# Optimization experiments

Hardware: AMD Instinct MI355X
Metric: run time of the kernel (lower is better)

## Reference

```python
import jax, jax.numpy as jnp
import numpy as np

H = 12          # num_attention_heads
HD = 64         # head_dim
GAMMA = 0.5
LOCAL_EPS = 0.8
N_APPROX = 7


def _l1norm(x, axis):
    # torch.nn.functional.normalize(x, p=1, dim=axis)
    n = jnp.sum(jnp.abs(x), axis=axis, keepdims=True)
    return x / jnp.maximum(n, 1e-12)


def setup_inputs() -> dict:
    key = jax.random.key(0)
    ks = jax.random.split(key, 6)
    B, S, E = 2, 512, 768
    std = 1.0 / np.sqrt(E)
    hidden_states = jax.random.normal(ks[0], (B, S, E), jnp.float32)
    Wq = jax.random.normal(ks[1], (E, E), jnp.float32) * std
    Wk = jax.random.normal(ks[2], (E, E), jnp.float32) * std
    Wv = jax.random.normal(ks[3], (E, E), jnp.float32) * std
    bq = jnp.zeros((E,), jnp.float32)
    bk = jnp.zeros((E,), jnp.float32)
    bv = jnp.zeros((E,), jnp.float32)
    g = jax.random.randint(ks[4], (B * S, B * S), 0, 2, jnp.int32)
    attention_mask = jnp.zeros((B, S), jnp.float32)
    return {"hidden_states": hidden_states, "Wq": Wq, "bq": bq, "Wk": Wk,
            "bk": bk, "Wv": Wv, "bv": bv, "g": g,
            "attention_mask": attention_mask}


def reference(hidden_states, Wq, bq, Wk, bk, Wv, bv, g, attention_mask):
    B, S, E = hidden_states.shape
    BN = B * S
    x = hidden_states  # torch flattens batch-major: token index = b*S + s
    q = (x @ Wq + bq) / jnp.sqrt(jnp.float32(HD))
    k = x @ Wk + bk
    v = x @ Wv + bv
    # [B,S,E] -> [BN,H,HD] -> [H,BN,HD]
    q = q.reshape(BN, H, HD).transpose(1, 0, 2)
    k = k.reshape(BN, H, HD).transpose(1, 0, 2)
    v = v.reshape(BN, H, HD).transpose(1, 0, 2)

    # W_G[h,i,j] = exp(k_i . q_j)
    W_G = jnp.exp(jnp.einsum('hid,hjd->hij', k, q))

    # sparsification mask combined with token mask
    bool_mask = (attention_mask >= 0).reshape(-1).astype(jnp.int32)  # [BN]
    g_eff = g * (bool_mask[:, None] * bool_mask[None, :])
    W_G = jnp.where(g_eff > 0, W_G, jnp.zeros((), W_G.dtype))

    out_degree = W_G.sum(axis=2)                       # [H, BN]
    rhos = jax.lax.stop_gradient(out_degree.max(axis=1))  # [H]

    eye = jnp.eye(BN, dtype=W_G.dtype)
    Bmat = rhos[:, None, None] * eye + W_G - out_degree[:, :, None] * eye

    B_power = jnp.broadcast_to(eye, (H, BN, BN))
    L_gamma = jnp.broadcast_to(eye, (H, BN, BN))
    num = 1.0
    den = jnp.ones((H,), W_G.dtype)
    for ii in range(1, N_APPROX + 1):  # fixed 7-term power series
        num = num * (GAMMA - ii + 1) * -1.0
        den = den * (ii * rhos)
        coef = num / den                               # [H]
        B_power = jnp.einsum('hij,hjk->hik', Bmat, B_power)
        L_gamma = L_gamma + coef[:, None, None] * B_power
    L_gamma = L_gamma * (rhos[:, None, None] ** GAMMA)
    diags = jnp.diagonal(L_gamma, axis1=-2, axis2=-1)  # [H, BN]
    L_gamma = _l1norm(diags[:, :, None] * eye - L_gamma, axis=2)

    attn = (LOCAL_EPS * jnp.einsum('hij,hjd->hid', _l1norm(W_G, 2), v)
            + (1.0 - LOCAL_EPS) * jnp.einsum('hij,hjd->hid', L_gamma, v))

    # faithful to torch: raw reshape of [H,BN,HD] into [B,S,H,HD]
    out = attn.reshape(B, S, H, HD)
    out = jnp.swapaxes(out, 0, 1).reshape(S, B, E)
    return jnp.swapaxes(out, 0, 1)
```

## Files before the change

### kernel.cpp

```cpp
#include <hip/hip_runtime.h>
#include <hip/hip_bf16.h>

typedef __attribute__((ext_vector_type(4))) float f32x4;
typedef __attribute__((ext_vector_type(8))) short s16x8;

typedef const __attribute__((address_space(1))) void* gptr_t;
typedef __attribute__((address_space(3))) void* lptr_t;

__device__ __forceinline__ short f2b(float f){ __hip_bfloat16 h=__float2bfloat16(f); return *(short*)&h; }
__device__ __forceinline__ float b2f(short s){ __hip_bfloat16 h; *(short*)&h = s; return __bfloat162float(h); }

__device__ __forceinline__ void gl_lds16(const void* g, void* l){
  __builtin_amdgcn_global_load_lds((gptr_t)g, (lptr_t)l, 16, 0, 0);
}


__global__ __launch_bounds__(256) void cvt_x(const float* __restrict__ X, short* __restrict__ Xb){
  int i = blockIdx.x*256 + threadIdx.x;
  const float4* p = (const float4*)(X + (size_t)i*8);
  float4 a = p[0], b = p[1];
  s16x8 o;
  o[0]=f2b(a.x); o[1]=f2b(a.y); o[2]=f2b(a.z); o[3]=f2b(a.w);
  o[4]=f2b(b.x); o[5]=f2b(b.y); o[6]=f2b(b.z); o[7]=f2b(b.w);
  *(s16x8*)(Xb + (size_t)i*8) = o;
}

__global__ __launch_bounds__(256) void cvt_wt(const float* __restrict__ W, short* __restrict__ WT){
  __shared__ short tile[64][72];
  int bl = blockIdx.x % 12, bn = blockIdx.x / 12;
  int l0 = bl*64, n0 = bn*64;
  int t = threadIdx.x;
  #pragma unroll
  for (int p=0;p<4;p++){
    int lr = p*16 + (t>>4);
    int nc = (t&15)*4;
    float4 v = *(const float4*)(W + (size_t)(l0+lr)*768 + n0 + nc);
    tile[lr][nc+0]=f2b(v.x); tile[lr][nc+1]=f2b(v.y); tile[lr][nc+2]=f2b(v.z); tile[lr][nc+3]=f2b(v.w);
  }
  __syncthreads();
  #pragma unroll
  for (int p=0;p<2;p++){
    int nr = p*32 + (t>>3);
    int lc = (t&7)*8;
    s16x8 o;
    #pragma unroll
    for(int u=0;u<8;u++) o[u] = tile[lc+u][nr];
    *(s16x8*)(WT + (size_t)(n0+nr)*768 + l0 + lc) = o;
  }
}

__global__ __launch_bounds__(256) void vtrans(const short* __restrict__ vs, short* __restrict__ vT){
  __shared__ short tile[64][72];
  int h = blockIdx.y; int i0 = blockIdx.x*64;
  int t = threadIdx.x;
  #pragma unroll
  for(int p=0;p<2;p++){
    int ir = p*32 + (t>>3); int c8=(t&7)*8;
    *(s16x8*)&tile[ir][c8] = *(const s16x8*)(vs + (size_t)(i0+ir)*768 + h*64 + c8);
  }
  __syncthreads();
  #pragma unroll
  for(int p=0;p<2;p++){
    int dr = p*32 + (t>>3); int i8=(t&7)*8;
    s16x8 o;
    #pragma unroll
    for(int u=0;u<8;u++) o[u]=tile[i8+u][dr];
    *(s16x8*)(vT + ((size_t)h*64 + dr)*1024 + i0 + i8) = o;
  }
}

__global__ __launch_bounds__(256) void qkv_gemm(const short* __restrict__ Xb, const short* __restrict__ WT,
      const float* __restrict__ bq, const float* __restrict__ bk, const float* __restrict__ bv,
      short* __restrict__ qs, short* __restrict__ ks, short* __restrict__ vs){
  __shared__ short lA[128*32], lB[128*32];
  int mat = blockIdx.y;
  const short* B = WT + (size_t)mat*768*768;
  const float* bias = mat==0?bq:(mat==1?bk:bv);
  short* outp = mat==0?qs:(mat==1?ks:vs);
  float scale = mat==0 ? 0.125f : 1.0f;
  int tm = (blockIdx.x / 6)*128, tn = (blockIdx.x % 6)*128;
  int t=threadIdx.x, wave=t>>6, lane=t&63;
  int srow=t>>2, scol=(t&3)*8;
  int wm=(wave>>1)*64, wn=(wave&1)*64;
  f32x4 acc[4][4]={};
  for (int k0=0;k0<768;k0+=32){
    #pragma unroll
    for(int r=0;r<2;++r){
      gl_lds16(Xb + (size_t)(tm+srow+r*64)*768 + k0 + scol, lA + r*2048 + wave*512);
      gl_lds16(B  + (size_t)(tn+srow+r*64)*768 + k0 + scol, lB + r*2048 + wave*512);
    }
    __syncthreads();
    int krow=(lane>>4)*8, rl=lane&15;
    s16x8 af[4], bfr[4];
    #pragma unroll
    for(int m=0;m<4;m++) af[m] = *(s16x8*)&lA[(wm+m*16+rl)*32 + krow];
    #pragma unroll
    for(int n=0;n<4;n++) bfr[n] = *(s16x8*)&lB[(wn+n*16+rl)*32 + krow];
    #pragma unroll
    for(int m=0;m<4;m++)
      #pragma unroll
      for(int n=0;n<4;n++)
        acc[m][n]=__builtin_amdgcn_mfma_f32_16x16x32_bf16(af[m],bfr[n],acc[m][n],0,0,0);
    __syncthreads();
  }
  int r0 = tm + wm + (lane>>4)*4, c0 = tn + wn + (lane&15);
  #pragma unroll
  for(int m=0;m<4;m++)
    #pragma unroll
    for(int n=0;n<4;n++){
      int col = c0 + n*16; float bb = bias[col];
      #pragma unroll
      for(int r=0;r<4;r++){
        int row = r0 + m*16 + r;
        outp[(size_t)row*768 + col] = f2b((acc[m][n][r] + bb)*scale);
      }
    }
}

__global__ __launch_bounds__(256) void wg_gemm(const short* __restrict__ kb, const short* __restrict__ qb,
      const int* __restrict__ g, const float* __restrict__ am,
      short* __restrict__ WG, float* __restrict__ od){
  __shared__ short lK[128*64], lQ[128*64];
  int h=blockIdx.y;
  int tm=(blockIdx.x>>3)*128, tn=(blockIdx.x&7)*128;
  int t=threadIdx.x, wave=t>>6, lane=t&63;
  int srow=t>>3, scol=(t&7)*8;
  int wm=(wave>>1)*64, wn=(wave&1)*64;
  #pragma unroll
  for(int r=0;r<4;++r){
    gl_lds16(kb + (size_t)(tm+srow+r*32)*768 + h*64 + scol, lK + r*2048 + wave*512);
    gl_lds16(qb + (size_t)(tn+srow+r*32)*768 + h*64 + scol, lQ + r*2048 + wave*512);
  }
  __syncthreads();
  int rl=lane&15;
  f32x4 acc[4][4]={};
  #pragma unroll
  for(int ks=0;ks<2;ks++){
    int krow=ks*32+(lane>>4)*8;
    s16x8 af[4], bfr[4];
    #pragma unroll
    for(int m=0;m<4;m++) af[m]=*(s16x8*)&lK[(wm+m*16+rl)*64+krow];
    #pragma unroll
    for(int n=0;n<4;n++) bfr[n]=*(s16x8*)&lQ[(wn+n*16+rl)*64+krow];
    #pragma unroll
    for(int m=0;m<4;m++)
      #pragma unroll
      for(int n=0;n<4;n++)
        acc[m][n]=__builtin_amdgcn_mfma_f32_16x16x32_bf16(af[m],bfr[n],acc[m][n],0,0,0);
  }
  size_t hm=(size_t)h<<20;
  int r0=tm+wm+(lane>>4)*4, c0=tn+wn+rl;
  #pragma unroll
  for(int m=0;m<4;m++){
    float rs[4]={0.f,0.f,0.f,0.f};
    #pragma unroll
    for(int n=0;n<4;n++){
      int col=c0+n*16;
      bool mc = am[col] >= 0.0f;
      #pragma unroll
      for(int r=0;r<4;r++){
        int row=r0+m*16+r;
        float e = expf(acc[m][n][r]);
        float w = (g[(size_t)row*1024+col]>0 && am[row]>=0.0f && mc) ? e : 0.f;
        WG[hm+(size_t)row*1024+col]=f2b(w);
        rs[r]+=w;
      }
    }
    #pragma unroll
    for(int r=0;r<4;r++){
      float s=rs[r];
      #pragma unroll
      for(int off=1;off<16;off<<=1) s+=__shfl_xor(s,off);
      if(rl==0) atomicAdd(&od[(h<<10)+r0+m*16+r], s);
    }
  }
}

__global__ void rhos_k(const float* __restrict__ od, float* __restrict__ rhos){
  __shared__ float red[256];
  int h = blockIdx.x, t = threadIdx.x;
  float m = -1e30f;
  for (int i=t;i<1024;i+=256) m = fmaxf(m, od[(h<<10)+i]);
  red[t]=m; __syncthreads();
  for(int s=128;s>0;s>>=1){ if(t<s) red[t]=fmaxf(red[t],red[t+s]); __syncthreads(); }
  if(t==0) rhos[h]=red[0];
}

__global__ __launch_bounds__(256) void amat_t(const short* __restrict__ WG, const float* __restrict__ od,
      const float* __restrict__ rhos, short* __restrict__ Am, short* __restrict__ AmT,
      short* __restrict__ T){
  __shared__ short tile[64][72];
  const float b7 = -33.f/2048.f, b6 = -21.f/1024.f;
  int h = blockIdx.y; int bx = blockIdx.x;
  int rb = bx >> 4, cb = bx & 15;
  int r0 = rb*64, c0 = cb*64;
  float rho = rhos[h]; float inv = 1.0f/fmaxf(rho,1e-30f);
  size_t hm = (size_t)h<<20;
  int t = threadIdx.x;
  #pragma unroll
  for(int p=0;p<2;p++){
    int r = p*32 + (t>>3); int c8 = (t&7)*8;
    size_t base = hm + (size_t)(r0+r)*1024 + c0 + c8;
    s16x8 w = *(const s16x8*)(WG + base);
    s16x8 oa, ot;
    float dadd = (rho - od[(h<<10)+r0+r])*inv;
    #pragma unroll
    for(int u=0;u<8;u++){
      bool dg = (rb==cb) && ((c8+u)==r);
      float a = b2f(w[u])*inv + (dg ? dadd : 0.f);
      oa[u]=f2b(a);
      ot[u]=f2b(b7*a + (dg ? b6 : 0.f));
      tile[r][c8+u]=oa[u];
    }
    *(s16x8*)(Am+base)=oa; *(s16x8*)(T+base)=ot;
  }
  __syncthreads();
  #pragma unroll
  for(int p=0;p<2;p++){
    int c = p*32 + (t>>3); int r8 = (t&7)*8;
    s16x8 o;
    #pragma unroll
    for(int u=0;u<8;u++) o[u]=tile[r8+u][c];
    *(s16x8*)(AmT + hm + (size_t)(c0+c)*1024 + r0 + r8) = o;
  }
}

#define GEMM2P_PROLOG \
  __shared__ short lA[2][4096], lB[2][4096]; \
  int wg = ((int)blockIdx.x & 7)*96 + ((int)blockIdx.x >> 3); \
  int h = wg >> 6; int tile = wg & 63; \
  int tm=(tile>>3)*128, tn=(tile&7)*128; \
  size_t hm=(size_t)h<<20; \
  const short* Ag = A + hm; const short* Bg = B + hm; \
  int t=threadIdx.x, wave=t>>6, lane=t&63; \
  int srow=t>>2, scol=(t&3)*8; \
  int wm=(wave>>1)*64, wn=(wave&1)*64; \
  int krow=(lane>>4)*8, rl=lane&15; \
  f32x4 acc[4][4]={}; \
  _Pragma("unroll") \
  for(int r=0;r<2;++r){ \
    gl_lds16(Ag + (size_t)(tm+srow+r*64)*1024 + scol, &lA[0][r*2048 + wave*512]); \
    gl_lds16(Bg + (size_t)(tn+srow+r*64)*1024 + scol, &lB[0][r*2048 + wave*512]); \
  } \
  __syncthreads(); \
  int cur=0; \
  _Pragma("unroll 1") \
  for(int k0=32;k0<1024;k0+=32){ \
    _Pragma("unroll") \
    for(int r=0;r<2;++r){ \
      gl_lds16(Ag + (size_t)(tm+srow+r*64)*1024 + k0 + scol, &lA[cur^1][r*2048 + wave*512]); \
      gl_lds16(Bg + (size_t)(tn+srow+r*64)*1024 + k0 + scol, &lB[cur^1][r*2048 + wave*512]); \
    } \
    s16x8 af[4], bfr[4]; \
    _Pragma("unroll") \
    for(int m=0;m<4;m++) af[m]=*(s16x8*)&lA[cur][(wm+m*16+rl)*32+krow]; \
    _Pragma("unroll") \
    for(int n=0;n<4;n++) bfr[n]=*(s16x8*)&lB[cur][(wn+n*16+rl)*32+krow]; \
    __builtin_amdgcn_s_setprio(1); \
    _Pragma("unroll") \
    for(int m=0;m<4;m++) \
      _Pragma("unroll") \
      for(int n=0;n<4;n++) \
        acc[m][n]=__builtin_amdgcn_mfma_f32_16x16x32_bf16(af[m],bfr[n],acc[m][n],0,0,0); \
    __builtin_amdgcn_s_setprio(0); \
    __syncthreads(); \
    cur^=1; \
  } \
  { s16x8 af[4], bfr[4]; \
    _Pragma("unroll") \
    for(int m=0;m<4;m++) af[m]=*(s16x8*)&lA[cur][(wm+m*16+rl)*32+krow]; \
    _Pragma("unroll") \
    for(int n=0;n<4;n++) bfr[n]=*(s16x8*)&lB[cur][(wn+n*16+rl)*32+krow]; \
    __builtin_amdgcn_s_setprio(1); \
    _Pragma("unroll") \
    for(int m=0;m<4;m++) \
      _Pragma("unroll") \
      for(int n=0;n<4;n++) \
        acc[m][n]=__builtin_amdgcn_mfma_f32_16x16x32_bf16(af[m],bfr[n],acc[m][n],0,0,0); \
    __builtin_amdgcn_s_setprio(0); \
  } \
  int r0=tm+wm+(lane>>4)*4, c0=tn+wn+(lane&15);

__global__ __launch_bounds__(256) void gemm2p_plain(const short* __restrict__ A, const short* __restrict__ B,
      short* __restrict__ D){
  GEMM2P_PROLOG
  short* Dg = D + hm;
  #pragma unroll
  for(int m=0;m<4;m++)
    #pragma unroll
    for(int n=0;n<4;n++){
      int col=c0+n*16;
      #pragma unroll
      for(int r=0;r<4;r++)
        Dg[(size_t)(r0+m*16+r)*1024 + col]=f2b(acc[m][n][r]);
    }
}

__global__ __launch_bounds__(256) void gemm2p_epi(const short* __restrict__ A, const short* __restrict__ B,
      short* __restrict__ D, const short* __restrict__ E1, const short* __restrict__ E2,
      float c0c, float cA, float cB){
  GEMM2P_PROLOG
  short* Dg = D + hm;
  const short* E1g = E1 + hm; const short* E2g = E2 + hm;
  #pragma unroll
  for(int m=0;m<4;m++)
    #pragma unroll
    for(int n=0;n<4;n++){
      int col=c0+n*16;
      #pragma unroll
      for(int r=0;r<4;r++){
        int row=r0+m*16+r;
        size_t e = (size_t)row*1024 + col;
        float v = acc[m][n][r] + cA*b2f(E1g[e]) + cB*b2f(E2g[e]);
        if(row==col) v += c0c;
        Dg[e]=f2b(v);
      }
    }
}

__global__ __launch_bounds__(256) void gemm2p_epi_stat(const short* __restrict__ A, const short* __restrict__ B,
      short* __restrict__ D, const short* __restrict__ E1, const short* __restrict__ E2,
      float c0c, float cA, float cB, float* __restrict__ rowabs, float* __restrict__ dvp){
  GEMM2P_PROLOG
  short* Dg = D + hm;
  const short* E1g = E1 + hm; const short* E2g = E2 + hm;
  #pragma unroll
  for(int m=0;m<4;m++){
    float rs[4]={0.f,0.f,0.f,0.f};
    #pragma unroll
    for(int n=0;n<4;n++){
      int col=c0+n*16;
      #pragma unroll
      for(int r=0;r<4;r++){
        int row=r0+m*16+r;
        size_t e = (size_t)row*1024 + col;
        float v = acc[m][n][r] + cA*b2f(E1g[e]) + cB*b2f(E2g[e]);
        if(row==col){ v += c0c; dvp[(h<<10)+row] = v; }
        rs[r] += fabsf(v);
        Dg[e]=f2b(v);
      }
    }
    #pragma unroll
    for(int r=0;r<4;r++){
      float s=rs[r];
      #pragma unroll
      for(int off=1;off<16;off<<=1) s+=__shfl_xor(s,off);
      if(rl==0) atomicAdd(&rowabs[(h<<10)+r0+m*16+r], s);
    }
  }
}

__global__ __launch_bounds__(256) void attn_k(const short* __restrict__ WG, const short* __restrict__ L,
    const short* __restrict__ vT, const short* __restrict__ vs,
    const float* __restrict__ od, const float* __restrict__ dv, const float* __restrict__ rowabs,
    float* __restrict__ out){
  __shared__ short lW[128*32], lL[128*32], lV[64*32];
  int h=blockIdx.y, tm=blockIdx.x*128;
  size_t hm=(size_t)h<<20;
  int t=threadIdx.x, wave=t>>6, lane=t&63;
  int srow=t>>2, scol=(t&3)*8;
  f32x4 a1[2][4]={}, a2[2][4]={};
  for(int j0=0;j0<1024;j0+=32){
    #pragma unroll
    for(int r=0;r<2;++r){
      gl_lds16(WG + hm + (size_t)(tm+srow+r*64)*1024 + j0 + scol, lW + r*2048 + wave*512);
      gl_lds16(L  + hm + (size_t)(tm+srow+r*64)*1024 + j0 + scol, lL + r*2048 + wave*512);
    }
    gl_lds16(vT + ((size_t)h*64 + srow)*1024 + j0 + scol, lV + wave*512);
    __syncthreads();
    int krow=(lane>>4)*8, rl=lane&15;
    s16x8 fw[2], fl[2], fv[4];
    #pragma unroll
    for(int m=0;m<2;m++){
      fw[m]=*(s16x8*)&lW[(wave*32+m*16+rl)*32+krow];
      fl[m]=*(s16x8*)&lL[(wave*32+m*16+rl)*32+krow];
    }
    #pragma unroll
    for(int n=0;n<4;n++) fv[n]=*(s16x8*)&lV[(n*16+rl)*32+krow];
    #pragma unroll
    for(int m=0;m<2;m++)
      #pragma unroll
      for(int n=0;n<4;n++){
        a1[m][n]=__builtin_amdgcn_mfma_f32_16x16x32_bf16(fw[m],fv[n],a1[m][n],0,0,0);
        a2[m][n]=__builtin_amdgcn_mfma_f32_16x16x32_bf16(fl[m],fv[n],a2[m][n],0,0,0);
      }
    __syncthreads();
  }
  #pragma unroll
  for(int m=0;m<2;m++)
    #pragma unroll
    for(int r=0;r<4;r++){
      int row = tm + wave*32 + m*16 + (lane>>4)*4 + r;
      float invod = 1.0f/fmaxf(od[(h<<10)+row], 1e-12f);
      float dvi = dv[(h<<10)+row];
      float ivr = 1.0f/fmaxf(rowabs[(h<<10)+row] - fabsf(dvi), 1e-12f);
      #pragma unroll
      for(int n=0;n<4;n++){
        int d = n*16 + (lane&15);
        float vv = b2f(vs[(size_t)row*768 + h*64 + d]);
        out[(((size_t)h<<10)+row)*64 + d] = 0.8f*a1[m][n][r]*invod + 0.2f*(dvi*vv - a2[m][n][r])*ivr;
      }
    }
}

extern "C" void kernel_launch(void* const* d_in, const int* in_sizes, int n_in,
                              void* d_out, int out_size, void* d_ws, size_t ws_size,
                              hipStream_t stream){
  const float* hs = (const float*)d_in[0];
  const float* Wq = (const float*)d_in[1];
  const float* bq = (const float*)d_in[2];
  const float* Wk = (const float*)d_in[3];
  const float* bk = (const float*)d_in[4];
  const float* Wv = (const float*)d_in[5];
  const float* bv = (const float*)d_in[6];
  const int*   g  = (const int*)d_in[7];
  const float* am = (const float*)d_in[8];
  float* out = (float*)d_out;

  char* w = (char*)d_ws;
  auto alloc=[&](size_t bytes)->char*{ char* p=w; w += (bytes+255)&~(size_t)255; return p; };
  short* Xb  = (short*)alloc((size_t)1024*768*2);
  short* WT  = (short*)alloc((size_t)3*768*768*2);
  short* qs  = (short*)alloc((size_t)1024*768*2);
  short* ks  = (short*)alloc((size_t)1024*768*2);
  short* vs  = (short*)alloc((size_t)1024*768*2);
  short* vT  = (short*)alloc((size_t)12*64*1024*2);
  short* WG  = (short*)alloc((size_t)12*1024*1024*2);
  short* Am  = (short*)alloc((size_t)12*1024*1024*2);
  short* AmT = (short*)alloc((size_t)12*1024*1024*2);
  short* Tm  = (short*)alloc((size_t)12*1024*1024*2);
  short* A2  = (short*)alloc((size_t)12*1024*1024*2);
  short* A3T = (short*)alloc((size_t)12*1024*1024*2);
  float* od  = (float*)alloc((size_t)12*1024*4);
  float* rh  = (float*)alloc((size_t)64*4);
  float* dv  = (float*)alloc((size_t)12*1024*4);
  float* rab = (float*)alloc((size_t)12*1024*4);

  hipMemsetAsync(od,  0, (size_t)12*1024*4, stream);
  hipMemsetAsync(rab, 0, (size_t)12*1024*4, stream);

  cvt_x<<<384,256,0,stream>>>(hs, Xb);
  cvt_wt<<<144,256,0,stream>>>(Wq, WT);
  cvt_wt<<<144,256,0,stream>>>(Wk, WT + (size_t)768*768);
  cvt_wt<<<144,256,0,stream>>>(Wv, WT + (size_t)2*768*768);
  qkv_gemm<<<dim3(48,3),256,0,stream>>>(Xb, WT, bq,bk,bv, qs,ks,vs);
  vtrans<<<dim3(16,12),256,0,stream>>>(vs, vT);
  wg_gemm<<<dim3(64,12),256,0,stream>>>(ks, qs, g, am, WG, od);
  rhos_k<<<12,256,0,stream>>>(od, rh);
  amat_t<<<dim3(256,12),256,0,stream>>>(WG, od, rh, Am, AmT, Tm);

  const float b1=-0.5f, b2=-0.125f, b3=-1.f/16.f, b4=-5.f/128.f, b5=-7.f/256.f;
  short* V = AmT;
  short* L = Tm;
  gemm2p_plain<<<768,256,0,stream>>>(Am, AmT, A2);
  gemm2p_plain<<<768,256,0,stream>>>(AmT, A2, A3T);
  gemm2p_epi<<<768,256,0,stream>>>(Tm, A3T, V, Am, A2, b3,b4,b5);
  gemm2p_epi_stat<<<768,256,0,stream>>>(V, A3T, L, Am, A2, 1.0f,b1,b2, rab, dv);

  attn_k<<<dim3(8,12),256,0,stream>>>(WG, L, vT, vs, od, dv, rab, out);
}
```

Before: 281.4 us.

## Load GEMM A operand directly to registers, stage only B through LDS

The four batched 1024x1024 GEMMs now load A-fragments straight from global memory into registers, double-buffered across k-steps, so only B goes through LDS. The main loop is unrolled by two with ping-pong register and LDS buffers. The aim is to halve LDS traffic and shared memory use, and LDS reads for A, at the cost of uncoalesced 16-byte global reads per lane and more registers. The WG kernel also switches expf to the fast __expf intrinsic.

```diff
diff --git a/kernel.cpp b/kernel.cpp
--- a/kernel.cpp
+++ b/kernel.cpp
@@ -160,7 +160,7 @@
       #pragma unroll
       for(int r=0;r<4;r++){
         int row=r0+m*16+r;
-        float e = expf(acc[m][n][r]);
+        float e = __expf(acc[m][n][r]);
         float w = (g[(size_t)row*1024+col]>0 && am[row]>=0.0f && mc) ? e : 0.f;
         WG[hm+(size_t)row*1024+col]=f2b(w);
         rs[r]+=w;
@@ -225,8 +225,29 @@
   }
 }
 
-#define GEMM2P_PROLOG \
-  __shared__ short lA[2][4096], lB[2][4096]; \
+#define GSTEP(AF, AFN, CUR, NXT, KN, DOPF) { \
+  if (DOPF) { \
+    _Pragma("unroll") \
+    for(int m_=0;m_<4;m_++) AFN[m_] = *(const s16x8*)(Arow[m_] + (KN)); \
+    _Pragma("unroll") \
+    for(int r_=0;r_<2;++r_) \
+      gl_lds16(Bg + (size_t)(tn+srow+r_*64)*1024 + (KN) + scol, &lB[NXT][r_*2048 + wave*512]); \
+  } \
+  s16x8 bfr[4]; \
+  _Pragma("unroll") \
+  for(int n_=0;n_<4;n_++) bfr[n_]=*(s16x8*)&lB[CUR][(wn+n_*16+rl)*32+krow]; \
+  __builtin_amdgcn_s_setprio(1); \
+  _Pragma("unroll") \
+  for(int m_=0;m_<4;m_++) \
+    _Pragma("unroll") \
+    for(int n_=0;n_<4;n_++) \
+      acc[m_][n_]=__builtin_amdgcn_mfma_f32_16x16x32_bf16(AF[m_],bfr[n_],acc[m_][n_],0,0,0); \
+  __builtin_amdgcn_s_setprio(0); \
+  __syncthreads(); \
+}
+
+#define GEMMA_PROLOG \
+  __shared__ short lB[2][4096]; \
   int wg = ((int)blockIdx.x & 7)*96 + ((int)blockIdx.x >> 3); \
   int h = wg >> 6; int tile = wg & 63; \
   int tm=(tile>>3)*128, tn=(tile&7)*128; \
@@ -236,54 +257,29 @@
   int srow=t>>2, scol=(t&3)*8; \
   int wm=(wave>>1)*64, wn=(wave&1)*64; \
   int krow=(lane>>4)*8, rl=lane&15; \
+  const short* Arow[4]; \
+  _Pragma("unroll") \
+  for(int m_=0;m_<4;m_++) Arow[m_] = Ag + (size_t)(tm+wm+m_*16+rl)*1024 + krow; \
   f32x4 acc[4][4]={}; \
+  s16x8 afA[4], afB[4]; \
   _Pragma("unroll") \
-  for(int r=0;r<2;++r){ \
-    gl_lds16(Ag + (size_t)(tm+srow+r*64)*1024 + scol, &lA[0][r*2048 + wave*512]); \
-    gl_lds16(Bg + (size_t)(tn+srow+r*64)*1024 + scol, &lB[0][r*2048 + wave*512]); \
+  for(int m_=0;m_<4;m_++) afA[m_] = *(const s16x8*)(Arow[m_]); \
+  _Pragma("unroll") \
+  for(int r_=0;r_<2;++r_) \
+    gl_lds16(Bg + (size_t)(tn+srow+r_*64)*1024 + scol, &lB[0][r_*2048 + wave*512]); \
+  __syncthreads(); \
+  _Pragma("unroll 1") \
+  for(int k0=0;k0<960;k0+=64){ \
+    GSTEP(afA, afB, 0, 1, k0+32, 1) \
+    GSTEP(afB, afA, 1, 0, k0+64, 1) \
   } \
-  __syncthreads(); \
-  int cur=0; \
-  _Pragma("unroll 1") \
-  for(int k0=32;k0<1024;k0+=32){ \
-    _Pragma("unroll") \
-    for(int r=0;r<2;++r){ \
-      gl_lds16(Ag + (size_t)(tm+srow+r*64)*1024 + k0 + scol, &lA[cur^1][r*2048 + wave*512]); \
-      gl_lds16(Bg + (size_t)(tn+srow+r*64)*1024 + k0 + scol, &lB[cur^1][r*2048 + wave*512]); \
-    } \
-    s16x8 af[4], bfr[4]; \
-    _Pragma("unroll") \
-    for(int m=0;m<4;m++) af[m]=*(s16x8*)&lA[cur][(wm+m*16+rl)*32+krow]; \
-    _Pragma("unroll") \
-    for(int n=0;n<4;n++) bfr[n]=*(s16x8*)&lB[cur][(wn+n*16+rl)*32+krow]; \
-    __builtin_amdgcn_s_setprio(1); \
-    _Pragma("unroll") \
-    for(int m=0;m<4;m++) \
-      _Pragma("unroll") \
-      for(int n=0;n<4;n++) \
-        acc[m][n]=__builtin_amdgcn_mfma_f32_16x16x32_bf16(af[m],bfr[n],acc[m][n],0,0,0); \
-    __builtin_amdgcn_s_setprio(0); \
-    __syncthreads(); \
-    cur^=1; \
-  } \
-  { s16x8 af[4], bfr[4]; \
-    _Pragma("unroll") \
-    for(int m=0;m<4;m++) af[m]=*(s16x8*)&lA[cur][(wm+m*16+rl)*32+krow]; \
-    _Pragma("unroll") \
-    for(int n=0;n<4;n++) bfr[n]=*(s16x8*)&lB[cur][(wn+n*16+rl)*32+krow]; \
-    __builtin_amdgcn_s_setprio(1); \
-    _Pragma("unroll") \
-    for(int m=0;m<4;m++) \
-      _Pragma("unroll") \
-      for(int n=0;n<4;n++) \
-        acc[m][n]=__builtin_amdgcn_mfma_f32_16x16x32_bf16(af[m],bfr[n],acc[m][n],0,0,0); \
-    __builtin_amdgcn_s_setprio(0); \
-  } \
+  GSTEP(afA, afB, 0, 1, 992, 1) \
+  GSTEP(afB, afA, 1, 0, 0, 0) \
   int r0=tm+wm+(lane>>4)*4, c0=tn+wn+(lane&15);
 
-__global__ __launch_bounds__(256) void gemm2p_plain(const short* __restrict__ A, const short* __restrict__ B,
+__global__ __launch_bounds__(256) void gemma_plain(const short* __restrict__ A, const short* __restrict__ B,
       short* __restrict__ D){
-  GEMM2P_PROLOG
+  GEMMA_PROLOG
   short* Dg = D + hm;
   #pragma unroll
   for(int m=0;m<4;m++)
@@ -296,10 +292,10 @@
     }
 }
 
-__global__ __launch_bounds__(256) void gemm2p_epi(const short* __restrict__ A, const short* __restrict__ B,
+__global__ __launch_bounds__(256) void gemma_epi(const short* __restrict__ A, const short* __restrict__ B,
       short* __restrict__ D, const short* __restrict__ E1, const short* __restrict__ E2,
       float c0c, float cA, float cB){
-  GEMM2P_PROLOG
+  GEMMA_PROLOG
   short* Dg = D + hm;
   const short* E1g = E1 + hm; const short* E2g = E2 + hm;
   #pragma unroll
@@ -318,10 +314,10 @@
     }
 }
 
-__global__ __launch_bounds__(256) void gemm2p_epi_stat(const short* __restrict__ A, const short* __restrict__ B,
+__global__ __launch_bounds__(256) void gemma_epi_stat(const short* __restrict__ A, const short* __restrict__ B,
       short* __restrict__ D, const short* __restrict__ E1, const short* __restrict__ E2,
       float c0c, float cA, float cB, float* __restrict__ rowabs, float* __restrict__ dvp){
-  GEMM2P_PROLOG
+  GEMMA_PROLOG
   short* Dg = D + hm;
   const short* E1g = E1 + hm; const short* E2g = E2 + hm;
   #pragma unroll
@@ -452,10 +448,10 @@
   const float b1=-0.5f, b2=-0.125f, b3=-1.f/16.f, b4=-5.f/128.f, b5=-7.f/256.f;
   short* V = AmT;
   short* L = Tm;
-  gemm2p_plain<<<768,256,0,stream>>>(Am, AmT, A2);
-  gemm2p_plain<<<768,256,0,stream>>>(AmT, A2, A3T);
-  gemm2p_epi<<<768,256,0,stream>>>(Tm, A3T, V, Am, A2, b3,b4,b5);
-  gemm2p_epi_stat<<<768,256,0,stream>>>(V, A3T, L, Am, A2, 1.0f,b1,b2, rab, dv);
+  gemma_plain<<<768,256,0,stream>>>(Am, AmT, A2);
+  gemma_plain<<<768,256,0,stream>>>(AmT, A2, A3T);
+  gemma_epi<<<768,256,0,stream>>>(Tm, A3T, V, Am, A2, b3,b4,b5);
+  gemma_epi_stat<<<768,256,0,stream>>>(V, A3T, L, Am, A2, 1.0f,b1,b2, rab, dv);
 
   attn_k<<<dim3(8,12),256,0,stream>>>(WG, L, vT, vs, od, dv, rab, out);
 }
```

After: 380.9 us. 1.35x slower.
